# Kernel optimization log

Measured on AMD Instinct MI355X. Metric: run time of the kernel, lower is better.

The kernel has to match this reference:

```python
import jax, jax.numpy as jnp
import numpy as np
from jax.scipy.special import logsumexp

B, S, H, T, M = 64, 512, 768, 500, 8
POSITION_WEIGHT = 0.6
LABEL_SMOOTH = 0.1
GAMMA = 2.0


def setup_inputs() -> dict:
    key = jax.random.key(0)
    ks = jax.random.split(key, 12)
    hidden = jax.random.normal(ks[0], (B, S, H), jnp.float32)  # BERT sequence_output stand-in
    lengths = jax.random.randint(ks[1], (B,), S // 2, S + 1)
    attention_mask = (jnp.arange(S)[None, :] < lengths[:, None]).astype(jnp.int32)
    position_labels = jax.random.randint(ks[2], (B, S), 0, 3).astype(jnp.int32)
    type_labels = jax.random.randint(ks[3], (B, M), 0, T).astype(jnp.int32)
    starts = jax.random.randint(ks[4], (B, M), 1, S // 2)
    ends = starts + jax.random.randint(ks[5], (B, M), 2, 8)
    valid = jax.random.uniform(ks[6], (B, M)) < 0.8  # some (batch, span) slots unused, like the original sum()>0 filter
    target_positions = jnp.where(valid[..., None], jnp.stack([starts, ends], -1), 0).astype(jnp.int32)
    # CRF params exactly as hardcoded in __init__
    trans = jnp.array([[-5.0, 20.0, -10000.0], [-50.0, 0.0, 50.0], [0.0, -50.0, 30.0]], jnp.float32)
    start_trans = jnp.array([0.0, 0.0, -10000.0], jnp.float32)
    end_trans = jnp.array([0.0, -100.0, 0.0], jnp.float32)
    return {
        'hidden': hidden,
        'attention_mask': attention_mask,
        'position_labels': position_labels,
        'type_labels': type_labels,
        'target_positions': target_positions,
        'bi_label_weight': jnp.asarray(0.5, jnp.float32),
        'W_pos': 0.02 * jax.random.normal(ks[7], (H, 3), jnp.float32),
        'b_pos': jnp.zeros((3,), jnp.float32),
        'start_trans': start_trans,
        'end_trans': end_trans,
        'trans': trans,
        'att_W1': 0.02 * jax.random.normal(ks[8], (H, 64), jnp.float32),
        'att_b1': jnp.zeros((64,), jnp.float32),
        'att_W2': 0.02 * jax.random.normal(ks[9], (64, 1), jnp.float32),
        'att_b2': jnp.zeros((1,), jnp.float32),
        'W_type': 0.02 * jax.random.normal(ks[10], (H, T), jnp.float32),
        'b_type': jnp.zeros((T,), jnp.float32),
    }


def crf_nll(em, labels, mask, start_trans, end_trans, trans):
    # torchcrf-style masked negative log-likelihood, reduction='none'
    maskf = mask.astype(em.dtype)
    emit = jnp.take_along_axis(em, labels[..., None], -1)[..., 0]  # [B,S]
    emit_score = (emit * maskf).sum(1)
    tr = trans[labels[:, :-1], labels[:, 1:]]  # [B,S-1]
    tr_score = (tr * maskf[:, 1:]).sum(1)
    last = mask.sum(1) - 1
    last_tags = jnp.take_along_axis(labels, last[:, None], 1)[:, 0]
    score = start_trans[labels[:, 0]] + emit_score + tr_score + end_trans[last_tags]
    # log partition via scan over time
    alpha = start_trans[None, :] + em[:, 0]  # [B,3]
    def step(alpha, xs):
        em_t, m_t = xs
        nxt = logsumexp(alpha[:, :, None] + trans[None, :, :] + em_t[:, None, :], axis=1)
        return jnp.where(m_t[:, None], nxt, alpha), None
    alpha, _ = jax.lax.scan(step, alpha, (em[:, 1:].transpose(1, 0, 2), mask[:, 1:].T))
    logZ = logsumexp(alpha + end_trans[None, :], axis=-1)
    return logZ - score  # = -log_likelihood


def reference(hidden, attention_mask, position_labels, type_labels, target_positions,
              bi_label_weight, W_pos, b_pos, start_trans, end_trans, trans,
              att_W1, att_b1, att_W2, att_b2, W_type, b_type):
    mask = attention_mask.astype(bool)
    emissions = hidden @ W_pos + b_pos  # [B,S,3]
    w = jnp.where(position_labels > 0, 1.0 + bi_label_weight, 1.0)[..., None]
    em_w = emissions * w
    position_loss = crf_nll(em_w, position_labels, mask, start_trans, end_trans, trans).mean()

    # span attention pooling, batched over all (B,M) pairs instead of the Python loop
    scores = (jnp.tanh(hidden @ att_W1 + att_b1) @ att_W2 + att_b2)[..., 0]  # [B,S]
    starts = target_positions[..., 0]
    ends = target_positions[..., 1]
    valid = target_positions.sum(-1) > 0  # [B,M]
    pos = jnp.arange(hidden.shape[1])
    span_mask = (pos[None, None, :] >= starts[..., None]) & (pos[None, None, :] < ends[..., None])  # [B,M,S]
    att = jnp.where(span_mask, scores[:, None, :], -1e9)
    aw = jax.nn.softmax(att, axis=-1)  # per-span softmax == softmax over the gathered span
    pooled = jnp.einsum('bms,bsh->bmh', aw, hidden)  # [B,M,H]
    logits = pooled @ W_type + b_type  # [B,M,T]

    # label-smoothed focal loss over valid spans only
    nT = logits.shape[-1]
    onehot = jax.nn.one_hot(type_labels, nT, dtype=logits.dtype)
    smooth = onehot * (1.0 - LABEL_SMOOTH) + LABEL_SMOOTH / nT
    logp = jax.nn.log_softmax(logits, axis=-1)
    probs = jnp.exp(logp)
    ce = -(smooth * logp).sum(-1)
    pt = (smooth * probs).sum(-1)
    focal = ce * (1.0 - pt) ** GAMMA
    v = valid.astype(focal.dtype)
    type_loss = (focal * v).sum() / jnp.maximum(v.sum(), 1.0) * 10.0

    joint = POSITION_WEIGHT * position_loss + (1.0 - POSITION_WEIGHT) * type_loss
    return jnp.stack([joint, position_loss, type_loss])
```

## Files before the change

### kernel.cpp

```cpp
#include <hip/hip_runtime.h>

#define L2E 1.44269504088896340736f
#define LN2 0.69314718055994530942f
#define NEGB -1e30f

typedef float f32x4 __attribute__((ext_vector_type(4)));
typedef __bf16 bf16x8 __attribute__((ext_vector_type(8)));

static constexpr size_t WT_ALL_OFF   = 0;
static constexpr size_t WT_TYPE_OFF  = 122880;
static constexpr size_t EM_T_OFF     = 909312;
static constexpr size_t SCORES_OFF   = 1302528;
static constexpr size_t LABELS_T_OFF = 1433600;
static constexpr size_t LEN_OFF      = 1564672;
static constexpr size_t POOLED_OFF   = 2351360;
static constexpr size_t MATM_OFF     = 3400192;
static constexpr size_t PSC_OFF      = 3547648;
static constexpr size_t PQ_OFF       = 3564032;
static constexpr size_t VL_OFF       = 3629568;

__device__ __forceinline__ unsigned short f2bf(float f) {
  unsigned u = __builtin_bit_cast(unsigned, f);
  u += 0x7FFFu + ((u >> 16) & 1u);
  return (unsigned short)(u >> 16);
}
__device__ __forceinline__ float sel3(float a, float b, float c, int i) {
  return i == 0 ? a : (i == 1 ? b : c);
}
__device__ __forceinline__ float lse3(float x, float y, float z) {
  float m = fmaxf(fmaxf(x, y), z);
  float p = exp2f((x - m) * L2E) + exp2f((y - m) * L2E) + exp2f((z - m) * L2E);
  return m + log2f(p) * LN2;
}
__device__ __forceinline__ bf16x8 pack8(float4 lo, float4 hi) {
  union { unsigned u[4]; bf16x8 v; } r;
  asm("v_cvt_pk_bf16_f32 %0, %1, %2" : "=v"(r.u[0]) : "v"(lo.x), "v"(lo.y));
  asm("v_cvt_pk_bf16_f32 %0, %1, %2" : "=v"(r.u[1]) : "v"(lo.z), "v"(lo.w));
  asm("v_cvt_pk_bf16_f32 %0, %1, %2" : "=v"(r.u[2]) : "v"(hi.x), "v"(hi.y));
  asm("v_cvt_pk_bf16_f32 %0, %1, %2" : "=v"(r.u[3]) : "v"(hi.z), "v"(hi.w));
  return r.v;
}
__device__ __forceinline__ void gload_lds16(const void* g, void* l) {
  __builtin_amdgcn_global_load_lds(
      (const __attribute__((address_space(1))) unsigned*)g,
      (__attribute__((address_space(3))) unsigned*)l, 16, 0, 0);
}

__global__ __launch_bounds__(256) void ka_prep(
    const float* __restrict__ W1, const float* __restrict__ Wpos,
    const float* __restrict__ Wtype, const int* __restrict__ amask,
    unsigned short* __restrict__ wt_all, unsigned short* __restrict__ wt_type,
    int* __restrict__ lengths) {
  const int bid = blockIdx.x, t = threadIdx.x;
  if (bid < 108) {
    __shared__ float tl[64][65];
    const bool is_type = bid < 96;
    const int kt = is_type ? (bid % 12) : (bid - 96);
    const int k0 = kt * 64;
    const int n0 = is_type ? (bid / 12) * 64 : 0;
    const int ld = is_type ? 500 : 64;
    const int nlim = is_type ? 500 : 64;
    const float* src = is_type ? Wtype : W1;
    unsigned short* dst = is_type ? wt_type : wt_all;
    const int n = t & 63;
    #pragma unroll
    for (int i = 0; i < 16; ++i) {
      int k = i * 4 + (t >> 6);
      tl[k][n] = (n0 + n < nlim) ? src[(size_t)(k0 + k) * ld + n0 + n] : 0.f;
    }
    __syncthreads();
    const int k = t & 63;
    #pragma unroll
    for (int i = 0; i < 16; ++i) {
      int nn = i * 4 + (t >> 6);
      dst[(size_t)(n0 + nn) * 768 + k0 + k] = f2bf(tl[k][nn]);
    }
  } else if (bid == 108) {
    for (int idx = t; idx < 16 * 768; idx += 256) {
      int n = 64 + idx / 768, k = idx % 768;
      float v = (n < 67) ? Wpos[k * 3 + (n - 64)] : 0.f;
      wt_all[(size_t)n * 768 + k] = f2bf(v);
    }
  } else {
    __shared__ int part[256];
    int bb = t >> 2, qq = t & 3;
    const int4* mp = (const int4*)(amask + bb * 512 + qq * 128);
    int s = 0;
    #pragma unroll 8
    for (int i = 0; i < 32; ++i) { int4 v = mp[i]; s += v.x + v.y + v.z + v.w; }
    part[t] = s;
    __syncthreads();
    if (qq == 0) lengths[bb] = part[t] + part[t + 1] + part[t + 2] + part[t + 3];
  }
}

__global__ __launch_bounds__(256) void k1_gemm(
    const float* __restrict__ hidden, const int* __restrict__ plab,
    const float* __restrict__ bpos, const float* __restrict__ b1,
    const float* __restrict__ W2, const float* __restrict__ b2,
    const float* __restrict__ biw, const unsigned short* __restrict__ wt_all,
    float* __restrict__ em_t, float* __restrict__ scores, int* __restrict__ labels_t) {
  __shared__ uint4 As[4][512];
  __shared__ uint4 Bs[4][512];
  const int t = threadIdx.x, w = t >> 6, l = t & 63;
  const int row0 = blockIdx.x * 64;
  const int c16 = l & 15, q = l >> 4;

  f32x4 acc[5];
  #pragma unroll
  for (int nt = 0; nt < 5; ++nt) acc[nt] = (f32x4){0.f, 0.f, 0.f, 0.f};

  auto stage = [&](int it) {
    const int bi = it & 3;
    const int k0 = it * 32;
    #pragma unroll
    for (int u = 0; u < 2; ++u) {
      int i = w * 128 + u * 64 + l;
      int row = i >> 3;
      int ss = (i & 7) ^ (row & 7);
      gload_lds16(hidden + (size_t)(row0 + row) * 768 + k0 + 4 * ss,
                  (void*)(As[bi] + (w * 128 + u * 64)));
    }
    #pragma unroll
    for (int u = 0; u < 2; ++u) {
      int i = w * 128 + u * 64 + l;
      int row = i >> 2;
      int ss = (i & 3) ^ ((row >> 1) & 3);
      gload_lds16(wt_all + (size_t)row * 768 + k0 + 8 * ss,
                  (void*)(Bs[bi] + (w * 128 + u * 64)));
    }
  };

  stage(0); stage(1);
  for (int it = 0; it < 24; ++it) {
    if (it < 22) stage(it + 2);
    if (it < 22)       asm volatile("s_waitcnt vmcnt(8)" ::: "memory");
    else if (it == 22) asm volatile("s_waitcnt vmcnt(4)" ::: "memory");
    else               asm volatile("s_waitcnt vmcnt(0)" ::: "memory");
    __builtin_amdgcn_s_barrier();
    __builtin_amdgcn_sched_barrier(0);

    const int bi = it & 3;
    const char* Ab = (const char*)As[bi];
    const char* Bb = (const char*)Bs[bi];
    const int arow = 16 * w + c16, r7 = arow & 7;
    float4 alo = *(const float4*)(Ab + arow * 128 + (((2 * q + 0) ^ r7) << 4));
    float4 ahi = *(const float4*)(Ab + arow * 128 + (((2 * q + 1) ^ r7) << 4));
    bf16x8 a = pack8(alo, ahi);
    #pragma unroll
    for (int nt = 0; nt < 5; ++nt) {
      const int brow = 16 * nt + c16;
      bf16x8 b = *(const bf16x8*)(Bb + brow * 64 + ((q ^ ((brow >> 1) & 3)) << 4));
      acc[nt] = __builtin_amdgcn_mfma_f32_16x16x32_bf16(a, b, acc[nt], 0, 0, 0);
    }
  }

  const float bias2 = b2[0];
  #pragma unroll
  for (int r = 0; r < 4; ++r) {
    float s = 0.f;
    #pragma unroll
    for (int nt = 0; nt < 4; ++nt) {
      int c = 16 * nt + c16;
      float x = acc[nt][r] + b1[c];
      float th = 1.f - 2.f / (1.f + exp2f(x * (2.f * L2E)));
      s += th * W2[c];
    }
    #pragma unroll
    for (int off = 1; off < 16; off <<= 1) s += __shfl_xor(s, off, 64);
    if (c16 == 0) {
      int row = row0 + 16 * w + 4 * q + r;
      scores[row] = s + bias2;
    }
  }
  if (c16 < 3) {
    const float bi = biw[0];
    #pragma unroll
    for (int r = 0; r < 4; ++r) {
      int row = row0 + 16 * w + 4 * q + r;
      int bb = row >> 9, ss = row & 511;
      int lab = plab[row];
      float wgt = (lab > 0) ? 1.f + bi : 1.f;
      float ev = (acc[4][r] + bpos[c16]) * wgt;
      em_t[(ss * 3 + c16) * 64 + bb] = ev;
      if (c16 == 0) labels_t[ss * 64 + bb] = lab;
    }
  }
}

__global__ __launch_bounds__(64) void kpc(
    const float* __restrict__ hidden, const float* __restrict__ scores,
    const int* __restrict__ tpos, unsigned short* __restrict__ pooled,
    const float* __restrict__ em_t, const int* __restrict__ labels_t,
    const int* __restrict__ lengths, const float* __restrict__ trans,
    float* __restrict__ matM, float* __restrict__ psc) {
  const int bid = blockIdx.x, l = threadIdx.x;
  if (bid < 512) {
    const int span = bid;
    const int b = span >> 3;
    const int st = tpos[span * 2], en = tpos[span * 2 + 1];
    int len = (st + en > 0) ? (en - st) : 0;
    float sv[7], aw[7];
    float wm = -1e30f;
    #pragma unroll
    for (int j = 0; j < 7; ++j) {
      sv[j] = (j < len) ? scores[b * 512 + st + j] : -1e30f;
      wm = fmaxf(wm, sv[j]);
    }
    float den = 0.f;
    #pragma unroll
    for (int j = 0; j < 7; ++j) {
      aw[j] = (j < len) ? exp2f((sv[j] - wm) * L2E) : 0.f;
      den += aw[j];
    }
    float inv = (den > 0.f) ? 1.f / den : 0.f;
    #pragma unroll
    for (int j = 0; j < 7; ++j) aw[j] *= inv;
    #pragma unroll
    for (int r = 0; r < 12; ++r) {
      int h = l + 64 * r;
      float acc = 0.f;
      #pragma unroll
      for (int j = 0; j < 7; ++j)
        if (j < len) acc += aw[j] * hidden[(size_t)(b * 512 + st + j) * 768 + h];
      pooled[span * 768 + h] = f2bf(acc);
    }
  } else {
    const int b = l, c = bid - 512;
    float T0 = trans[0], T1 = trans[1], T2 = trans[2];
    float T3 = trans[3], T4 = trans[4], T5 = trans[5];
    float T6 = trans[6], T7 = trans[7], T8 = trans[8];
    const int L = lengths[b];
    const int s0 = 8 * c;
    int labp = labels_t[(c ? (s0 - 1) : 0) * 64 + b];

    float E0[8], E1[8], E2[8]; int LB[8];
    #pragma unroll
    for (int i = 0; i < 8; ++i) {
      E0[i] = em_t[((s0 + i) * 3 + 0) * 64 + b];
      E1[i] = em_t[((s0 + i) * 3 + 1) * 64 + b];
      E2[i] = em_t[((s0 + i) * 3 + 2) * 64 + b];
      LB[i] = labels_t[(s0 + i) * 64 + b];
    }
    float M[9];
    #pragma unroll
    for (int i = 0; i < 9; ++i) M[i] = (i == 0 || i == 4 || i == 8) ? 0.f : NEGB;
    float sc = 0.f;
    #pragma unroll
    for (int i = 0; i < 8; ++i) {
      int s = s0 + i;
      bool act = (s >= 1) && (s < L);
      float N[9];
      #pragma unroll
      for (int r = 0; r < 3; ++r) {
        float ma = M[3 * r], mb = M[3 * r + 1], mc = M[3 * r + 2];
        N[3 * r + 0] = lse3(ma + T0, mb + T3, mc + T6) + E0[i];
        N[3 * r + 1] = lse3(ma + T1, mb + T4, mc + T7) + E1[i];
        N[3 * r + 2] = lse3(ma + T2, mb + T5, mc + T8) + E2[i];
      }
      #pragma unroll
      for (int r = 0; r < 9; ++r) M[r] = act ? N[r] : M[r];
      int lab = LB[i];
      float ev = sel3(E0[i], E1[i], E2[i], lab);
      float trv = sel3(sel3(T0, T1, T2, lab),
                       sel3(T3, T4, T5, lab),
                       sel3(T6, T7, T8, lab), labp);
      sc += act ? (ev + trv) : 0.f;
      labp = lab;
    }
    #pragma unroll
    for (int i = 0; i < 9; ++i) matM[(c * 9 + i) * 64 + b] = M[i];
    psc[c * 64 + b] = sc;
  }
}

__global__ __launch_bounds__(256) void k_tg2(
    const unsigned short* __restrict__ pooled, const unsigned short* __restrict__ wt_type,
    const float* __restrict__ btype, const int* __restrict__ tlab,
    float* __restrict__ pq, float* __restrict__ vlbuf) {
  __shared__ unsigned short Apool[8][776];
  __shared__ uint4 Bt[6][512];
  __shared__ float logitsL[8][68];
  const int t = threadIdx.x, w = t >> 6, l = t & 63;
  const int b = blockIdx.x >> 3, oc = blockIdx.x & 7;
  const int c16 = l & 15, q = l >> 4;

  #pragma unroll
  for (int u = 0; u < 3; ++u) {
    int i = u * 256 + t;
    int row = i / 96, c8 = i % 96;
    *(uint4*)(&Apool[row][c8 * 8]) =
        *(const uint4*)(pooled + (size_t)(b * 8 + row) * 768 + c8 * 8);
  }

  auto stageB = [&](int kt) {
    const int bi = kt % 6;
    #pragma unroll
    for (int u = 0; u < 2; ++u) {
      int i = u * 256 + t;
      int row = i >> 3;
      int ss = (i & 7) ^ (row & 7);
      gload_lds16(wt_type + (size_t)(oc * 64 + row) * 768 + kt * 64 + 8 * ss,
                  (void*)(Bt[bi] + i));
    }
  };

  stageB(0); stageB(1); stageB(2);
  f32x4 acc = (f32x4){0.f, 0.f, 0.f, 0.f};
  const bf16x8 zerov = (bf16x8)(__bf16)0.f;
  for (int kt = 0; kt < 12; ++kt) {
    if (kt < 9)        { stageB(kt + 3); asm volatile("s_waitcnt vmcnt(6)" ::: "memory"); }
    else if (kt == 9)  asm volatile("s_waitcnt vmcnt(4)" ::: "memory");
    else if (kt == 10) asm volatile("s_waitcnt vmcnt(2)" ::: "memory");
    else               asm volatile("s_waitcnt vmcnt(0)" ::: "memory");
    __builtin_amdgcn_s_barrier();
    __builtin_amdgcn_sched_barrier(0);

    const char* Bb = (const char*)Bt[kt % 6];
    const int brow = 16 * w + c16, r7 = brow & 7;
    #pragma unroll
    for (int ks = 0; ks < 2; ++ks) {
      bf16x8 a = (c16 < 8) ? *(const bf16x8*)(&Apool[c16][kt * 64 + ks * 32 + 8 * q]) : zerov;
      bf16x8 bb = *(const bf16x8*)(Bb + brow * 128 + (((ks * 4 + q) ^ r7) << 4));
      acc = __builtin_amdgcn_mfma_f32_16x16x32_bf16(a, bb, acc, 0, 0, 0);
    }
  }
  if (q < 2) {
    #pragma unroll
    for (int r = 0; r < 4; ++r) logitsL[4 * q + r][16 * w + c16] = acc[r];
  }
  __syncthreads();

  #pragma unroll
  for (int rr = 0; rr < 2; ++rr) {
    const int row = 2 * w + rr;
    int gc = 64 * oc + l;
    bool ok = gc < 500;
    float lv = ok ? logitsL[row][l] + btype[gc] : -1e30f;
    float m = lv;
    #pragma unroll
    for (int off = 1; off < 64; off <<= 1) m = fmaxf(m, __shfl_xor(m, off, 64));
    float se = ok ? exp2f((lv - m) * L2E) : 0.f;
    float ss = ok ? lv : 0.f;
    #pragma unroll
    for (int off = 1; off < 64; off <<= 1) {
      se += __shfl_xor(se, off, 64);
      ss += __shfl_xor(ss, off, 64);
    }
    if (l == 0) {
      int grow = b * 8 + row;
      float* dst = pq + ((size_t)grow * 8 + oc) * 4;
      dst[0] = m; dst[1] = se; dst[2] = ss;
      int lbl = tlab[grow];
      if ((lbl >> 6) == oc) vlbuf[grow] = logitsL[row][lbl & 63] + btype[lbl];
    }
  }
}

__global__ __launch_bounds__(256) void k_final(
    const float* __restrict__ pq, const float* __restrict__ vlbuf,
    const int* __restrict__ tpos, const float* __restrict__ em_t,
    const int* __restrict__ labels_t, const int* __restrict__ lengths,
    const float* __restrict__ strans, const float* __restrict__ etrans,
    const float* __restrict__ matM, const float* __restrict__ psc,
    float* __restrict__ out) {
  __shared__ float red[16];
  const int t = threadIdx.x, w = t >> 6, l = t & 63;

  float fsum = 0.f, vsum = 0.f;
  #pragma unroll
  for (int rr = 0; rr < 2; ++rr) {
    int row = t + 256 * rr;
    const float* p0 = pq + (size_t)row * 32;
    float gm = -1e30f;
    #pragma unroll
    for (int o = 0; o < 8; ++o) gm = fmaxf(gm, p0[4 * o]);
    float se = 0.f, ss = 0.f;
    #pragma unroll
    for (int o = 0; o < 8; ++o) {
      se += p0[4 * o + 1] * exp2f((p0[4 * o] - gm) * L2E);
      ss += p0[4 * o + 2];
    }
    float logZ = gm + log2f(se) * LN2;
    float lp = vlbuf[row] - logZ;
    float ce = -(0.9f * lp + 2e-4f * (ss - 500.f * logZ));
    float pt = 0.9f * exp2f(lp * L2E) + 2e-4f;
    float focal = ce * (1.f - pt) * (1.f - pt);
    bool valid = (tpos[row * 2] + tpos[row * 2 + 1]) > 0;
    fsum += valid ? focal : 0.f;
    vsum += valid ? 1.f : 0.f;
  }
  #pragma unroll
  for (int off = 1; off < 64; off <<= 1) {
    fsum += __shfl_xor(fsum, off, 64);
    vsum += __shfl_xor(vsum, off, 64);
  }
  if (l == 0) { red[w * 2] = fsum; red[w * 2 + 1] = vsum; }
  __syncthreads();
  if (t == 0) {
    red[8] = red[0] + red[2] + red[4] + red[6];
    red[9] = red[1] + red[3] + red[5] + red[7];
  }
  __syncthreads();

  if (t < 64) {
    const int b = t;
    const int L = lengths[b];
    const float st0 = strans[0], st1 = strans[1], st2 = strans[2];
    const float et0 = etrans[0], et1 = etrans[1], et2 = etrans[2];
    float e00 = em_t[0 * 64 + b], e01 = em_t[1 * 64 + b], e02 = em_t[2 * 64 + b];
    int lab0 = labels_t[b];
    float a0 = st0 + e00, a1 = st1 + e01, a2 = st2 + e02;
    float score = sel3(st0, st1, st2, lab0) + sel3(e00, e01, e02, lab0);

    float cur[4][10];
    #pragma unroll
    for (int j = 0; j < 4; ++j) {
      #pragma unroll
      for (int i = 0; i < 9; ++i) cur[j][i] = matM[(j * 9 + i) * 64 + b];
      cur[j][9] = psc[j * 64 + b];
    }
    for (int r = 0; r < 16; ++r) {
      float nxt[4][10];
      if (r < 15) {
        #pragma unroll
        for (int j = 0; j < 4; ++j) {
          int c = (r + 1) * 4 + j;
          #pragma unroll
          for (int i = 0; i < 9; ++i) nxt[j][i] = matM[(c * 9 + i) * 64 + b];
          nxt[j][9] = psc[c * 64 + b];
        }
      }
      #pragma unroll
      for (int j = 0; j < 4; ++j) {
        float n0 = lse3(a0 + cur[j][0], a1 + cur[j][3], a2 + cur[j][6]);
        float n1 = lse3(a0 + cur[j][1], a1 + cur[j][4], a2 + cur[j][7]);
        float n2 = lse3(a0 + cur[j][2], a1 + cur[j][5], a2 + cur[j][8]);
        a0 = n0; a1 = n1; a2 = n2;
        score += cur[j][9];
      }
      if (r < 15) {
        #pragma unroll
        for (int j = 0; j < 4; ++j)
          #pragma unroll
          for (int i = 0; i < 10; ++i) cur[j][i] = nxt[j][i];
      }
    }
    int last = labels_t[(L - 1) * 64 + b];
    score += sel3(et0, et1, et2, last);
    float logZ = lse3(a0 + et0, a1 + et1, a2 + et2);
    float nll = logZ - score;
    #pragma unroll
    for (int off = 1; off < 64; off <<= 1) nll += __shfl_xor(nll, off, 64);
    if (b == 0) {
      float pos = nll / 64.f;
      float type = red[8] / fmaxf(red[9], 1.f) * 10.f;
      out[0] = 0.6f * pos + 0.4f * type;
      out[1] = pos;
      out[2] = type;
    }
  }
}

extern "C" void kernel_launch(void* const* d_in, const int* in_sizes, int n_in,
                              void* d_out, int out_size, void* d_ws, size_t ws_size,
                              hipStream_t stream) {
  const float* hidden = (const float*)d_in[0];
  const int*   amask  = (const int*)d_in[1];
  const int*   plab   = (const int*)d_in[2];
  const int*   tlab   = (const int*)d_in[3];
  const int*   tpos   = (const int*)d_in[4];
  const float* biw    = (const float*)d_in[5];
  const float* Wpos   = (const float*)d_in[6];
  const float* bpos   = (const float*)d_in[7];
  const float* strans = (const float*)d_in[8];
  const float* etrans = (const float*)d_in[9];
  const float* trans  = (const float*)d_in[10];
  const float* W1     = (const float*)d_in[11];
  const float* b1     = (const float*)d_in[12];
  const float* W2     = (const float*)d_in[13];
  const float* b2     = (const float*)d_in[14];
  const float* Wtype  = (const float*)d_in[15];
  const float* btype  = (const float*)d_in[16];
  float* out = (float*)d_out;
  char* ws = (char*)d_ws;

  unsigned short* wt_all  = (unsigned short*)(ws + WT_ALL_OFF);
  unsigned short* wt_type = (unsigned short*)(ws + WT_TYPE_OFF);
  float* em_t    = (float*)(ws + EM_T_OFF);
  float* scores  = (float*)(ws + SCORES_OFF);
  int*   labelsT = (int*)(ws + LABELS_T_OFF);
  int*   lengths = (int*)(ws + LEN_OFF);
  unsigned short* pooled = (unsigned short*)(ws + POOLED_OFF);
  float* matM    = (float*)(ws + MATM_OFF);
  float* psc     = (float*)(ws + PSC_OFF);
  float* pq      = (float*)(ws + PQ_OFF);
  float* vlbuf   = (float*)(ws + VL_OFF);

  ka_prep<<<110, 256, 0, stream>>>(W1, Wpos, Wtype, amask, wt_all, wt_type, lengths);
  k1_gemm<<<512, 256, 0, stream>>>(hidden, plab, bpos, b1, W2, b2, biw, wt_all,
                                   em_t, scores, labelsT);
  kpc<<<576, 64, 0, stream>>>(hidden, scores, tpos, pooled, em_t, labelsT, lengths,
                              trans, matM, psc);
  k_tg2<<<512, 256, 0, stream>>>(pooled, wt_type, btype, tlab, pq, vlbuf);
  k_final<<<1, 256, 0, stream>>>(pq, vlbuf, tpos, em_t, labelsT, lengths,
                                 strans, etrans, matM, psc, out);
}
```

Before: 85.83 us.

## Fuse final reduction into type GEMM via last-block counter and move Wtype prep

Moves the W_type transpose/bf16 conversion out of the prep kernel into the pooling/CRF-chunk kernel, so the small prep kernel launches fewer blocks ahead of the main GEMM. Repacks the pooling and CRF-chunk work into 256-thread blocks with four waves each. Folds the single-block final reduction into the type-GEMM kernel using an atomic counter, so the last finishing block runs the CRF scan and writes the output, which removes one kernel launch. The cost is atomics and thread fences, plus one block doing a serial tail at the end.

Result: slower. 95.28 us (+11.0%).

```diff
diff --git a/kernel.cpp b/kernel.cpp
--- a/kernel.cpp
+++ b/kernel.cpp
@@ -14,6 +14,7 @@
 static constexpr size_t LABELS_T_OFF = 1433600;
 static constexpr size_t LEN_OFF      = 1564672;
 static constexpr size_t POOLED_OFF   = 2351360;
+static constexpr size_t CNT_OFF      = 3399936;
 static constexpr size_t MATM_OFF     = 3400192;
 static constexpr size_t PSC_OFF      = 3547648;
 static constexpr size_t PQ_OFF       = 3564032;
@@ -48,34 +49,26 @@
 
 __global__ __launch_bounds__(256) void ka_prep(
     const float* __restrict__ W1, const float* __restrict__ Wpos,
-    const float* __restrict__ Wtype, const int* __restrict__ amask,
-    unsigned short* __restrict__ wt_all, unsigned short* __restrict__ wt_type,
-    int* __restrict__ lengths) {
+    const int* __restrict__ amask, unsigned short* __restrict__ wt_all,
+    int* __restrict__ lengths, unsigned* __restrict__ cnt) {
   const int bid = blockIdx.x, t = threadIdx.x;
-  if (bid < 108) {
+  if (bid < 12) {
     __shared__ float tl[64][65];
-    const bool is_type = bid < 96;
-    const int kt = is_type ? (bid % 12) : (bid - 96);
-    const int k0 = kt * 64;
-    const int n0 = is_type ? (bid / 12) * 64 : 0;
-    const int ld = is_type ? 500 : 64;
-    const int nlim = is_type ? 500 : 64;
-    const float* src = is_type ? Wtype : W1;
-    unsigned short* dst = is_type ? wt_type : wt_all;
+    const int k0 = bid * 64;
     const int n = t & 63;
     #pragma unroll
     for (int i = 0; i < 16; ++i) {
       int k = i * 4 + (t >> 6);
-      tl[k][n] = (n0 + n < nlim) ? src[(size_t)(k0 + k) * ld + n0 + n] : 0.f;
+      tl[k][n] = W1[(size_t)(k0 + k) * 64 + n];
     }
     __syncthreads();
     const int k = t & 63;
     #pragma unroll
     for (int i = 0; i < 16; ++i) {
       int nn = i * 4 + (t >> 6);
-      dst[(size_t)(n0 + nn) * 768 + k0 + k] = f2bf(tl[k][nn]);
-    }
-  } else if (bid == 108) {
+      wt_all[(size_t)nn * 768 + k0 + k] = f2bf(tl[k][nn]);
+    }
+  } else if (bid == 12) {
     for (int idx = t; idx < 16 * 768; idx += 256) {
       int n = 64 + idx / 768, k = idx % 768;
       float v = (n < 67) ? Wpos[k * 3 + (n - 64)] : 0.f;
@@ -91,6 +84,7 @@
     part[t] = s;
     __syncthreads();
     if (qq == 0) lengths[bb] = part[t] + part[t + 1] + part[t + 2] + part[t + 3];
+    if (t == 0) *cnt = 0u;
   }
 }
 
@@ -188,15 +182,17 @@
   }
 }
 
-__global__ __launch_bounds__(64) void kpc(
+__global__ __launch_bounds__(256) void kpc2(
     const float* __restrict__ hidden, const float* __restrict__ scores,
     const int* __restrict__ tpos, unsigned short* __restrict__ pooled,
     const float* __restrict__ em_t, const int* __restrict__ labels_t,
     const int* __restrict__ lengths, const float* __restrict__ trans,
+    const float* __restrict__ Wtype, unsigned short* __restrict__ wt_type,
     float* __restrict__ matM, float* __restrict__ psc) {
-  const int bid = blockIdx.x, l = threadIdx.x;
-  if (bid < 512) {
-    const int span = bid;
+  const int bid = blockIdx.x, t = threadIdx.x, w = t >> 6, l = t & 63;
+
+  if (bid < 128) {
+    const int span = bid * 4 + w;
     const int b = span >> 3;
     const int st = tpos[span * 2], en = tpos[span * 2 + 1];
     int len = (st + en > 0) ? (en - st) : 0;
@@ -225,8 +221,8 @@
         if (j < len) acc += aw[j] * hidden[(size_t)(b * 512 + st + j) * 768 + h];
       pooled[span * 768 + h] = f2bf(acc);
     }
-  } else {
-    const int b = l, c = bid - 512;
+  } else if (bid < 144) {
+    const int b = l, c = (bid - 128) * 4 + w;
     float T0 = trans[0], T1 = trans[1], T2 = trans[2];
     float T3 = trans[3], T4 = trans[4], T5 = trans[5];
     float T6 = trans[6], T7 = trans[7], T8 = trans[8];
@@ -271,16 +267,41 @@
     #pragma unroll
     for (int i = 0; i < 9; ++i) matM[(c * 9 + i) * 64 + b] = M[i];
     psc[c * 64 + b] = sc;
-  }
-}
-
-__global__ __launch_bounds__(256) void k_tg2(
+  } else {
+    __shared__ float tl[64][65];
+    const int tb = bid - 144;
+    const int k0 = (tb % 12) * 64;
+    const int n0 = (tb / 12) * 64;
+    const int n = t & 63;
+    #pragma unroll
+    for (int i = 0; i < 16; ++i) {
+      int k = i * 4 + (t >> 6);
+      tl[k][n] = (n0 + n < 500) ? Wtype[(size_t)(k0 + k) * 500 + n0 + n] : 0.f;
+    }
+    __syncthreads();
+    const int k = t & 63;
+    #pragma unroll
+    for (int i = 0; i < 16; ++i) {
+      int nn = i * 4 + (t >> 6);
+      wt_type[(size_t)(n0 + nn) * 768 + k0 + k] = f2bf(tl[k][nn]);
+    }
+  }
+}
+
+__global__ __launch_bounds__(256) void k_tg3(
     const unsigned short* __restrict__ pooled, const unsigned short* __restrict__ wt_type,
     const float* __restrict__ btype, const int* __restrict__ tlab,
-    float* __restrict__ pq, float* __restrict__ vlbuf) {
+    const int* __restrict__ tpos, const float* __restrict__ em_t,
+    const int* __restrict__ labels_t, const int* __restrict__ lengths,
+    const float* __restrict__ strans, const float* __restrict__ etrans,
+    const float* __restrict__ matM, const float* __restrict__ psc,
+    float* __restrict__ pq, float* __restrict__ vlbuf,
+    unsigned* __restrict__ cnt, float* __restrict__ out) {
   __shared__ unsigned short Apool[8][776];
   __shared__ uint4 Bt[6][512];
   __shared__ float logitsL[8][68];
+  __shared__ float red[16];
+  __shared__ int last_flag;
   const int t = threadIdx.x, w = t >> 6, l = t & 63;
   const int b = blockIdx.x >> 3, oc = blockIdx.x & 7;
   const int c16 = l & 15, q = l >> 4;
@@ -355,17 +376,16 @@
       if ((lbl >> 6) == oc) vlbuf[grow] = logitsL[row][lbl & 63] + btype[lbl];
     }
   }
-}
-
-__global__ __launch_bounds__(256) void k_final(
-    const float* __restrict__ pq, const float* __restrict__ vlbuf,
-    const int* __restrict__ tpos, const float* __restrict__ em_t,
-    const int* __restrict__ labels_t, const int* __restrict__ lengths,
-    const float* __restrict__ strans, const float* __restrict__ etrans,
-    const float* __restrict__ matM, const float* __restrict__ psc,
-    float* __restrict__ out) {
-  __shared__ float red[16];
-  const int t = threadIdx.x, w = t >> 6, l = t & 63;
+
+  __syncthreads();
+  if (t == 0) {
+    __threadfence();
+    unsigned old = atomicAdd(cnt, 1u);
+    last_flag = (old == 511u);
+  }
+  __syncthreads();
+  if (!last_flag) return;
+  __threadfence();
 
   float fsum = 0.f, vsum = 0.f;
   #pragma unroll
@@ -404,12 +424,12 @@
   __syncthreads();
 
   if (t < 64) {
-    const int b = t;
-    const int L = lengths[b];
+    const int b2_ = t;
+    const int L = lengths[b2_];
     const float st0 = strans[0], st1 = strans[1], st2 = strans[2];
     const float et0 = etrans[0], et1 = etrans[1], et2 = etrans[2];
-    float e00 = em_t[0 * 64 + b], e01 = em_t[1 * 64 + b], e02 = em_t[2 * 64 + b];
-    int lab0 = labels_t[b];
+    float e00 = em_t[0 * 64 + b2_], e01 = em_t[1 * 64 + b2_], e02 = em_t[2 * 64 + b2_];
+    int lab0 = labels_t[b2_];
     float a0 = st0 + e00, a1 = st1 + e01, a2 = st2 + e02;
     float score = sel3(st0, st1, st2, lab0) + sel3(e00, e01, e02, lab0);
 
@@ -417,8 +437,8 @@
     #pragma unroll
     for (int j = 0; j < 4; ++j) {
       #pragma unroll
-      for (int i = 0; i < 9; ++i) cur[j][i] = matM[(j * 9 + i) * 64 + b];
-      cur[j][9] = psc[j * 64 + b];
+      for (int i = 0; i < 9; ++i) cur[j][i] = matM[(j * 9 + i) * 64 + b2_];
+      cur[j][9] = psc[j * 64 + b2_];
     }
     for (int r = 0; r < 16; ++r) {
       float nxt[4][10];
@@ -427,8 +447,8 @@
         for (int j = 0; j < 4; ++j) {
           int c = (r + 1) * 4 + j;
           #pragma unroll
-          for (int i = 0; i < 9; ++i) nxt[j][i] = matM[(c * 9 + i) * 64 + b];
-          nxt[j][9] = psc[c * 64 + b];
+          for (int i = 0; i < 9; ++i) nxt[j][i] = matM[(c * 9 + i) * 64 + b2_];
+          nxt[j][9] = psc[c * 64 + b2_];
         }
       }
       #pragma unroll
@@ -446,13 +466,13 @@
           for (int i = 0; i < 10; ++i) cur[j][i] = nxt[j][i];
       }
     }
-    int last = labels_t[(L - 1) * 64 + b];
+    int last = labels_t[(L - 1) * 64 + b2_];
     score += sel3(et0, et1, et2, last);
     float logZ = lse3(a0 + et0, a1 + et1, a2 + et2);
     float nll = logZ - score;
     #pragma unroll
     for (int off = 1; off < 64; off <<= 1) nll += __shfl_xor(nll, off, 64);
-    if (b == 0) {
+    if (b2_ == 0) {
       float pos = nll / 64.f;
       float type = red[8] / fmaxf(red[9], 1.f) * 10.f;
       out[0] = 0.6f * pos + 0.4f * type;
@@ -492,17 +512,17 @@
   int*   labelsT = (int*)(ws + LABELS_T_OFF);
   int*   lengths = (int*)(ws + LEN_OFF);
   unsigned short* pooled = (unsigned short*)(ws + POOLED_OFF);
+  unsigned* cnt  = (unsigned*)(ws + CNT_OFF);
   float* matM    = (float*)(ws + MATM_OFF);
   float* psc     = (float*)(ws + PSC_OFF);
   float* pq      = (float*)(ws + PQ_OFF);
   float* vlbuf   = (float*)(ws + VL_OFF);
 
-  ka_prep<<<110, 256, 0, stream>>>(W1, Wpos, Wtype, amask, wt_all, wt_type, lengths);
+  ka_prep<<<14, 256, 0, stream>>>(W1, Wpos, amask, wt_all, lengths, cnt);
   k1_gemm<<<512, 256, 0, stream>>>(hidden, plab, bpos, b1, W2, b2, biw, wt_all,
                                    em_t, scores, labelsT);
-  kpc<<<576, 64, 0, stream>>>(hidden, scores, tpos, pooled, em_t, labelsT, lengths,
-                              trans, matM, psc);
-  k_tg2<<<512, 256, 0, stream>>>(pooled, wt_type, btype, tlab, pq, vlbuf);
-  k_final<<<1, 256, 0, stream>>>(pq, vlbuf, tpos, em_t, labelsT, lengths,
-                                 strans, etrans, matM, psc, out);
-}
+  kpc2<<<240, 256, 0, stream>>>(hidden, scores, tpos, pooled, em_t, labelsT, lengths,
+                                trans, Wtype, wt_type, matM, psc);
+  k_tg3<<<512, 256, 0, stream>>>(pooled, wt_type, btype, tlab, tpos, em_t, labelsT,
+                                 lengths, strans, etrans, matM, psc, pq, vlbuf, cnt, out);
+}
```

## Split GEMM N-tiles across two wave groups with 512-thread blocks

Applied to the files above, without the earlier changes.

The hidden-projection GEMM now runs 8 waves per block instead of 4. Each M-tile's five N-tiles are split 3/2 between two wave groups, and the partial attention scores are combined through shared memory. Each thread now issues one async load per operand per stage, with the vmcnt waits adjusted to match. The goal is more waves for latency hiding and shorter MFMA chains per wave, at the cost of an extra block barrier, a shared-memory reduction and an uneven split of work between the two groups.

Measured after the change: 86.06 us, median of 3. No clear change (+0.3%).

```diff
diff --git a/kernel.cpp b/kernel.cpp
--- a/kernel.cpp
+++ b/kernel.cpp
@@ -94,7 +94,7 @@
   }
 }
 
-__global__ __launch_bounds__(256) void k1_gemm(
+__global__ __launch_bounds__(512) void k1_gemm(
     const float* __restrict__ hidden, const int* __restrict__ plab,
     const float* __restrict__ bpos, const float* __restrict__ b1,
     const float* __restrict__ W2, const float* __restrict__ b2,
@@ -102,40 +102,30 @@
     float* __restrict__ em_t, float* __restrict__ scores, int* __restrict__ labels_t) {
   __shared__ uint4 As[4][512];
   __shared__ uint4 Bs[4][512];
+  __shared__ float sp[64][2];
   const int t = threadIdx.x, w = t >> 6, l = t & 63;
   const int row0 = blockIdx.x * 64;
   const int c16 = l & 15, q = l >> 4;
-
-  f32x4 acc[5];
+  const int m = w & 3, g = w >> 2;
+
+  f32x4 acc[3];
   #pragma unroll
-  for (int nt = 0; nt < 5; ++nt) acc[nt] = (f32x4){0.f, 0.f, 0.f, 0.f};
+  for (int j = 0; j < 3; ++j) acc[j] = (f32x4){0.f, 0.f, 0.f, 0.f};
 
   auto stage = [&](int it) {
     const int bi = it & 3;
     const int k0 = it * 32;
-    #pragma unroll
-    for (int u = 0; u < 2; ++u) {
-      int i = w * 128 + u * 64 + l;
-      int row = i >> 3;
-      int ss = (i & 7) ^ (row & 7);
-      gload_lds16(hidden + (size_t)(row0 + row) * 768 + k0 + 4 * ss,
-                  (void*)(As[bi] + (w * 128 + u * 64)));
-    }
-    #pragma unroll
-    for (int u = 0; u < 2; ++u) {
-      int i = w * 128 + u * 64 + l;
-      int row = i >> 2;
-      int ss = (i & 3) ^ ((row >> 1) & 3);
-      gload_lds16(wt_all + (size_t)row * 768 + k0 + 8 * ss,
-                  (void*)(Bs[bi] + (w * 128 + u * 64)));
-    }
+    { int row = t >> 3, ss = (t & 7) ^ (row & 7);
+      gload_lds16(hidden + (size_t)(row0 + row) * 768 + k0 + 4 * ss, (void*)(As[bi] + t)); }
+    { int row = t >> 2, ss = (t & 3) ^ ((row >> 1) & 3);
+      gload_lds16(wt_all + (size_t)row * 768 + k0 + 8 * ss, (void*)(Bs[bi] + t)); }
   };
 
   stage(0); stage(1);
   for (int it = 0; it < 24; ++it) {
     if (it < 22) stage(it + 2);
-    if (it < 22)       asm volatile("s_waitcnt vmcnt(8)" ::: "memory");
-    else if (it == 22) asm volatile("s_waitcnt vmcnt(4)" ::: "memory");
+    if (it < 22)       asm volatile("s_waitcnt vmcnt(4)" ::: "memory");
+    else if (it == 22) asm volatile("s_waitcnt vmcnt(2)" ::: "memory");
     else               asm volatile("s_waitcnt vmcnt(0)" ::: "memory");
     __builtin_amdgcn_s_barrier();
     __builtin_amdgcn_sched_barrier(0);
@@ -143,45 +133,66 @@
     const int bi = it & 3;
     const char* Ab = (const char*)As[bi];
     const char* Bb = (const char*)Bs[bi];
-    const int arow = 16 * w + c16, r7 = arow & 7;
+    const int arow = 16 * m + c16, r7 = arow & 7;
     float4 alo = *(const float4*)(Ab + arow * 128 + (((2 * q + 0) ^ r7) << 4));
     float4 ahi = *(const float4*)(Ab + arow * 128 + (((2 * q + 1) ^ r7) << 4));
     bf16x8 a = pack8(alo, ahi);
-    #pragma unroll
-    for (int nt = 0; nt < 5; ++nt) {
-      const int brow = 16 * nt + c16;
-      bf16x8 b = *(const bf16x8*)(Bb + brow * 64 + ((q ^ ((brow >> 1) & 3)) << 4));
-      acc[nt] = __builtin_amdgcn_mfma_f32_16x16x32_bf16(a, b, acc[nt], 0, 0, 0);
-    }
-  }
-
-  const float bias2 = b2[0];
+    if (g == 0) {
+      #pragma unroll
+      for (int j = 0; j < 3; ++j) {
+        const int brow = 16 * j + c16;
+        bf16x8 b = *(const bf16x8*)(Bb + brow * 64 + ((q ^ ((brow >> 1) & 3)) << 4));
+        acc[j] = __builtin_amdgcn_mfma_f32_16x16x32_bf16(a, b, acc[j], 0, 0, 0);
+      }
+    } else {
+      #pragma unroll
+      for (int j = 0; j < 2; ++j) {
+        const int brow = 16 * (3 + j) + c16;
+        bf16x8 b = *(const bf16x8*)(Bb + brow * 64 + ((q ^ ((brow >> 1) & 3)) << 4));
+        acc[j] = __builtin_amdgcn_mfma_f32_16x16x32_bf16(a, b, acc[j], 0, 0, 0);
+      }
+    }
+  }
+
   #pragma unroll
   for (int r = 0; r < 4; ++r) {
     float s = 0.f;
-    #pragma unroll
-    for (int nt = 0; nt < 4; ++nt) {
-      int c = 16 * nt + c16;
-      float x = acc[nt][r] + b1[c];
+    if (g == 0) {
+      #pragma unroll
+      for (int j = 0; j < 3; ++j) {
+        int c = 16 * j + c16;
+        float x = acc[j][r] + b1[c];
+        float th = 1.f - 2.f / (1.f + exp2f(x * (2.f * L2E)));
+        s += th * W2[c];
+      }
+    } else {
+      int c = 48 + c16;
+      float x = acc[0][r] + b1[c];
       float th = 1.f - 2.f / (1.f + exp2f(x * (2.f * L2E)));
-      s += th * W2[c];
+      s = th * W2[c];
     }
     #pragma unroll
     for (int off = 1; off < 16; off <<= 1) s += __shfl_xor(s, off, 64);
-    if (c16 == 0) {
-      int row = row0 + 16 * w + 4 * q + r;
-      scores[row] = s + bias2;
-    }
-  }
-  if (c16 < 3) {
+    if (c16 == 0) sp[16 * m + 4 * q + r][g] = s;
+  }
+  __syncthreads();
+
+  if (g == 0) {
+    const float bias2 = b2[0];
+    #pragma unroll
+    for (int r = 0; r < 4; ++r) {
+      int row = 16 * m + 4 * q + r;
+      if (c16 == 0) scores[row0 + row] = sp[row][0] + sp[row][1] + bias2;
+    }
+  } else if (c16 < 3) {
     const float bi = biw[0];
     #pragma unroll
     for (int r = 0; r < 4; ++r) {
-      int row = row0 + 16 * w + 4 * q + r;
+      int row = row0 + 16 * m + 4 * q + r;
       int bb = row >> 9, ss = row & 511;
       int lab = plab[row];
       float wgt = (lab > 0) ? 1.f + bi : 1.f;
-      float ev = (acc[4][r] + bpos[c16]) * wgt;
+      float ev = (acc[1][r] + bpos[c16]) * wgt;
       em_t[(ss * 3 + c16) * 64 + bb] = ev;
       if (c16 == 0) labels_t[ss * 64 + bb] = lab;
     }
@@ -498,7 +509,7 @@
   float* vlbuf   = (float*)(ws + VL_OFF);
 
   ka_prep<<<110, 256, 0, stream>>>(W1, Wpos, Wtype, amask, wt_all, wt_type, lengths);
-  k1_gemm<<<512, 256, 0, stream>>>(hidden, plab, bpos, b1, W2, b2, biw, wt_all,
+  k1_gemm<<<512, 512, 0, stream>>>(hidden, plab, bpos, b1, W2, b2, biw, wt_all,
                                    em_t, scores, labelsT);
   kpc<<<576, 64, 0, stream>>>(hidden, scores, tpos, pooled, em_t, labelsT, lengths,
                               trans, matM, psc);
```
